# Optimization experiments

Hardware: AMD Instinct MI355X
Metric: run time of the kernel (lower is better)

## Reference

```python
import jax, jax.numpy as jnp
import numpy as np

B, L1, L2, D = 32, 512, 512, 1024


def setup_inputs() -> dict:
    key = jax.random.key(0)
    k1, k2, k3, k4 = jax.random.split(key, 4)
    v1 = jax.random.normal(k1, (B, L1, D), dtype=jnp.float32)
    v2 = jax.random.normal(k2, (B, L2, D), dtype=jnp.float32)
    # row/column is fully masked (which would NaN the softmax).
    v1_mask = jax.random.uniform(k3, (B, L1)) < 0.2
    v2_mask = jax.random.uniform(k4, (B, L2)) < 0.2
    return {"v1": v1, "v2": v2, "v1_mask": v1_mask, "v2_mask": v2_mask}


def reference(v1, v2, v1_mask, v2_mask):
    # similarity: [B, L1, L2]
    sim = jnp.einsum("bid,bjd->bij", v1, v2)
    neg_inf = jnp.float32(-jnp.inf)
    # softmax over v2 positions (dim=2), masking padded v2 columns
    v1_v2_attn = jax.nn.softmax(
        jnp.where(v2_mask[:, None, :], neg_inf, sim), axis=2)
    # softmax over v1 positions (dim=1), masking padded v1 rows
    v2_v1_attn = jax.nn.softmax(
        jnp.where(v1_mask[:, :, None], neg_inf, sim), axis=1)
    attended_v1 = jnp.einsum("bij,bjd->bid", v1_v2_attn, v2)  # [B,L1,D]
    attended_v2 = jnp.einsum("bij,bid->bjd", v2_v1_attn, v1)  # [B,L2,D]
    attended_v1 = jnp.where(v1_mask[:, :, None], 0.0, attended_v1)
    attended_v2 = jnp.where(v2_mask[:, :, None], 0.0, attended_v2)
    return attended_v1, attended_v2
```

## Files before the change

### kernel.cpp

```cpp
#include <hip/hip_runtime.h>
#include <stdint.h>


#define Bn 32
#define Ln 512
#define Dn 1024

typedef __attribute__((ext_vector_type(4))) float f32x4;
typedef __attribute__((ext_vector_type(4))) unsigned short u16x4;
typedef __attribute__((ext_vector_type(8))) unsigned short u16x8;
typedef __attribute__((ext_vector_type(8))) __bf16 bf16x8;

union bfcast { u16x8 u; bf16x8 b; };

__device__ __forceinline__ unsigned short f2bf(float f) {
  unsigned int u = __float_as_uint(f);
  u += 0x7FFFu + ((u >> 16) & 1u);
  return (unsigned short)(u >> 16);
}

__device__ __forceinline__ void async_cp16(const void* g, void* l) {
  __builtin_amdgcn_global_load_lds(
      (__attribute__((address_space(1))) void*)(g),
      (__attribute__((address_space(3))) void*)(l), 16, 0, 0);
}

__device__ __forceinline__ void cvt8(f32x4 x0, f32x4 x1,
                                     bf16x8* hi, bf16x8* lo) {
  float xs[8] = {x0[0], x0[1], x0[2], x0[3], x1[0], x1[1], x1[2], x1[3]};
  u16x8 h, l;
#pragma unroll
  for (int e = 0; e < 8; e++) {
    unsigned int u = __float_as_uint(xs[e]);
    h[e] = (unsigned short)(u >> 16);
    float hf = __uint_as_float(u & 0xFFFF0000u);
    l[e] = (unsigned short)(__float_as_uint(xs[e] - hf) >> 16);
  }
  bfcast ch, cl;
  ch.u = h; cl.u = l;
  *hi = ch.b; *lo = cl.b;
}

__global__ __launch_bounds__(256) void conv_t(
    const float* __restrict__ v1, const float* __restrict__ v2,
    unsigned short* __restrict__ v1t, unsigned short* __restrict__ v2t) {
  __shared__ float tile[64][65];
  const int z = blockIdx.z;
  const float* src = (z < Bn) ? v1 : v2;
  unsigned short* dt = (z < Bn) ? v1t : v2t;
  const int b = z & 31;
  const int d0 = blockIdx.x << 6;
  const int l0 = blockIdx.y << 6;
  const int tid = threadIdx.x;
#pragma unroll
  for (int it = 0; it < 4; it++) {
    int lin = (it << 8) + tid;
    int l = lin >> 4;
    int d4 = (lin & 15) << 2;
    f32x4 x = *(const f32x4*)(src + (size_t)(b * Ln + l0 + l) * Dn + d0 + d4);
    tile[l][d4] = x[0]; tile[l][d4 + 1] = x[1];
    tile[l][d4 + 2] = x[2]; tile[l][d4 + 3] = x[3];
  }
  __syncthreads();
#pragma unroll
  for (int it = 0; it < 4; it++) {
    int lin = (it << 8) + tid;
    int d = lin >> 4;
    int l4 = (lin & 15) << 2;
    u16x4 o;
    o[0] = f2bf(tile[l4][d]);     o[1] = f2bf(tile[l4 + 1][d]);
    o[2] = f2bf(tile[l4 + 2][d]); o[3] = f2bf(tile[l4 + 3][d]);
    *(u16x4*)(dt + (size_t)(b * Dn + d0 + d) * Ln + l0 + l4) = o;
  }
}

__global__ __launch_bounds__(256) void sim_gemm_split(
    const float* __restrict__ V1, const float* __restrict__ V2,
    float* __restrict__ C) {
  __shared__ float As[128 * 32];
  __shared__ float Bs[128 * 32];
  const int b = blockIdx.z;
  const float* Ab = V1 + (size_t)b * Ln * Dn;
  const float* Bb = V2 + (size_t)b * Ln * Dn;
  float* Cb = C + (size_t)b * Ln * Ln;
  const int m0 = blockIdx.y << 7;
  const int n0 = blockIdx.x << 7;
  const int tid = threadIdx.x;
  const int lane = tid & 63;
  const int wave = tid >> 6;
  const int wrow = (wave >> 1) << 6;
  const int wcol = (wave & 1) << 6;

  const int srow = lane >> 3;
  const int scol = ((lane & 7) ^ srow) << 2;
  const float* ga = Ab + (size_t)(m0 + (wave << 5) + srow) * Dn + scol;
  const float* gb = Bb + (size_t)(n0 + (wave << 5) + srow) * Dn + scol;

  const int r = lane & 15;
  const int q = lane >> 4;

  const f32x4 zero4 = {0.f, 0.f, 0.f, 0.f};
  f32x4 acc[4][4];
#pragma unroll
  for (int i = 0; i < 4; i++)
#pragma unroll
    for (int j = 0; j < 4; j++) acc[i][j] = zero4;

  for (int k0 = 0; k0 < Dn; k0 += 32) {
    __syncthreads();
#pragma unroll
    for (int j = 0; j < 4; j++) {
      async_cp16(ga + k0 + j * 8 * Dn, As + ((wave << 5) + j * 8) * 32);
      async_cp16(gb + k0 + j * 8 * Dn, Bs + ((wave << 5) + j * 8) * 32);
    }
    __syncthreads();
    bf16x8 ah[4], al[4], bh[4], bl[4];
#pragma unroll
    for (int t = 0; t < 4; t++) {
      int ra = wrow + (t << 4) + r;
      f32x4 x0 = *(const f32x4*)(As + ra * 32 + ((((q << 1)    ) ^ (ra & 7)) << 2));
      f32x4 x1 = *(const f32x4*)(As + ra * 32 + ((((q << 1) | 1) ^ (ra & 7)) << 2));
      cvt8(x0, x1, &ah[t], &al[t]);
      int rb = wcol + (t << 4) + r;
      f32x4 y0 = *(const f32x4*)(Bs + rb * 32 + ((((q << 1)    ) ^ (rb & 7)) << 2));
      f32x4 y1 = *(const f32x4*)(Bs + rb * 32 + ((((q << 1) | 1) ^ (rb & 7)) << 2));
      cvt8(y0, y1, &bh[t], &bl[t]);
    }
#pragma unroll
    for (int tm = 0; tm < 4; tm++)
#pragma unroll
      for (int tn = 0; tn < 4; tn++) {
        acc[tm][tn] = __builtin_amdgcn_mfma_f32_16x16x32_bf16(
            ah[tm], bh[tn], acc[tm][tn], 0, 0, 0);
        acc[tm][tn] = __builtin_amdgcn_mfma_f32_16x16x32_bf16(
            ah[tm], bl[tn], acc[tm][tn], 0, 0, 0);
        acc[tm][tn] = __builtin_amdgcn_mfma_f32_16x16x32_bf16(
            al[tm], bh[tn], acc[tm][tn], 0, 0, 0);
      }
  }

#pragma unroll
  for (int tm = 0; tm < 4; tm++) {
    int rowb = m0 + wrow + (tm << 4) + (q << 2);
#pragma unroll
    for (int reg = 0; reg < 4; reg++) {
      int row = rowb + reg;
#pragma unroll
      for (int tn = 0; tn < 4; tn++) {
        int col = n0 + wcol + (tn << 4) + r;
        Cb[(size_t)row * Ln + col] = acc[tm][tn][reg];
      }
    }
  }
}

__global__ __launch_bounds__(256) void gemm_nt(
    const unsigned short* __restrict__ A, const unsigned short* __restrict__ Bm,
    float* __restrict__ C, const int* __restrict__ rowmask,
    int M, int N, int K) {
  __shared__ unsigned short As[128 * 32];
  __shared__ unsigned short Bs[128 * 32];
  const int b = blockIdx.z;
  const unsigned short* Ab = A + (size_t)b * M * K;
  const unsigned short* Bb = Bm + (size_t)b * N * K;
  float* Cb = C + (size_t)b * M * N;
  const int m0 = blockIdx.y << 7;
  const int n0 = blockIdx.x << 7;
  const int tid = threadIdx.x;
  const int lane = tid & 63;
  const int wave = tid >> 6;
  const int wrow = (wave >> 1) << 6;
  const int wcol = (wave & 1) << 6;

  const int srow = tid >> 2;
  const int skof = (tid & 3) << 3;
  const unsigned short* ga0 = Ab + (size_t)(m0 + srow) * K + skof;
  const unsigned short* ga1 = Ab + (size_t)(m0 + 64 + srow) * K + skof;
  const unsigned short* gb0 = Bb + (size_t)(n0 + srow) * K + skof;
  const unsigned short* gb1 = Bb + (size_t)(n0 + 64 + srow) * K + skof;

  const int r = lane & 15;
  const int q = lane >> 4;

  const f32x4 zero4 = {0.f, 0.f, 0.f, 0.f};
  f32x4 acc[4][4];
#pragma unroll
  for (int i = 0; i < 4; i++)
#pragma unroll
    for (int j = 0; j < 4; j++) acc[i][j] = zero4;

  for (int k0 = 0; k0 < K; k0 += 32) {
    __syncthreads();
    async_cp16(ga0 + k0, As + (wave << 9));
    async_cp16(ga1 + k0, As + 2048 + (wave << 9));
    async_cp16(gb0 + k0, Bs + (wave << 9));
    async_cp16(gb1 + k0, Bs + 2048 + (wave << 9));
    __syncthreads();
    bf16x8 af[4], bf[4];
#pragma unroll
    for (int t = 0; t < 4; t++) {
      af[t] = *(const bf16x8*)(As + ((wrow + (t << 4) + r) << 5) + (q << 3));
      bf[t] = *(const bf16x8*)(Bs + ((wcol + (t << 4) + r) << 5) + (q << 3));
    }
#pragma unroll
    for (int tm = 0; tm < 4; tm++)
#pragma unroll
      for (int tn = 0; tn < 4; tn++)
        acc[tm][tn] = __builtin_amdgcn_mfma_f32_16x16x32_bf16(
            af[tm], bf[tn], acc[tm][tn], 0, 0, 0);
  }

  const int* mb = rowmask ? rowmask + b * M : (const int*)0;
#pragma unroll
  for (int tm = 0; tm < 4; tm++) {
    int rowb = m0 + wrow + (tm << 4) + (q << 2);
#pragma unroll
    for (int reg = 0; reg < 4; reg++) {
      int row = rowb + reg;
      float mz = (mb && mb[row]) ? 0.f : 1.f;
#pragma unroll
      for (int tn = 0; tn < 4; tn++) {
        int col = n0 + wcol + (tn << 4) + r;
        Cb[(size_t)row * N + col] = acc[tm][tn][reg] * mz;
      }
    }
  }
}

__global__ __launch_bounds__(256) void row_softmax(
    const float* __restrict__ sim, const int* __restrict__ v2m,
    unsigned short* __restrict__ A1) {
  const int row = (blockIdx.x << 2) + (threadIdx.x >> 6);
  const int lane = threadIdx.x & 63;
  const int b = row >> 9;
  const float* s = sim + (size_t)row * Ln;
  const int* mk = v2m + (b << 9);
  const float NEGINF = -__builtin_inff();
  float v[8];
  float mx = NEGINF;
#pragma unroll
  for (int t = 0; t < 8; t++) {
    int j = lane + (t << 6);
    float x = mk[j] ? NEGINF : s[j];
    v[t] = x;
    mx = fmaxf(mx, x);
  }
#pragma unroll
  for (int off = 32; off > 0; off >>= 1) mx = fmaxf(mx, __shfl_xor(mx, off));
  float sum = 0.f;
#pragma unroll
  for (int t = 0; t < 8; t++) {
    float e = (v[t] > NEGINF) ? __expf(v[t] - mx) : 0.f;
    v[t] = e;
    sum += e;
  }
#pragma unroll
  for (int off = 32; off > 0; off >>= 1) sum += __shfl_xor(sum, off);
  float rs = 1.f / sum;
  unsigned short* o = A1 + (size_t)row * Ln;
#pragma unroll
  for (int t = 0; t < 8; t++) o[lane + (t << 6)] = f2bf(v[t] * rs);
}

__global__ __launch_bounds__(256) void csm_part(
    const float* __restrict__ sim, const int* __restrict__ v1m,
    float* __restrict__ pmax, float* __restrict__ psum) {
  __shared__ float sm[4][64], ss[4][64];
  const int b = blockIdx.z;
  const int ic = blockIdx.y;
  const int i0 = ic << 6;
  const int j0 = blockIdx.x << 6;
  const int tx = threadIdx.x & 63;
  const int ty = threadIdx.x >> 6;
  const float* S = sim + (size_t)b * (Ln * Ln) + j0 + tx;
  const int* mk = v1m + (b << 9) + i0;
  const float NEGINF = -__builtin_inff();
  float x[16];
#pragma unroll
  for (int k = 0; k < 16; k++) {
    int il = (k << 2) + ty;
    float v = S[(size_t)(i0 + il) * Ln];
    x[k] = mk[il] ? NEGINF : v;
  }
  float m = NEGINF;
#pragma unroll
  for (int k = 0; k < 16; k++) m = fmaxf(m, x[k]);
  float s = 0.f;
#pragma unroll
  for (int k = 0; k < 16; k++) s += (x[k] > NEGINF) ? __expf(x[k] - m) : 0.f;
  sm[ty][tx] = m;
  ss[ty][tx] = s;
  __syncthreads();
  if (ty == 0) {
    float M = fmaxf(fmaxf(sm[0][tx], sm[1][tx]), fmaxf(sm[2][tx], sm[3][tx]));
    float Sv = 0.f;
#pragma unroll
    for (int p = 0; p < 4; p++)
      Sv += (sm[p][tx] > NEGINF) ? ss[p][tx] * __expf(sm[p][tx] - M) : 0.f;
    int idx = (((b << 3) + ic) << 9) + j0 + tx;
    pmax[idx] = M;
    psum[idx] = Sv;
  }
}

__global__ __launch_bounds__(256) void csm_comb(
    const float* __restrict__ pmax, const float* __restrict__ psum,
    float* __restrict__ cmax, float* __restrict__ crs) {
  const int col = (blockIdx.x << 8) + threadIdx.x;
  const int b = col >> 9;
  const int j = col & 511;
  const float NEGINF = -__builtin_inff();
  float mm[8], sv[8];
#pragma unroll
  for (int p = 0; p < 8; p++) {
    int idx = (((b << 3) + p) << 9) + j;
    mm[p] = pmax[idx];
    sv[p] = psum[idx];
  }
  float M = NEGINF;
#pragma unroll
  for (int p = 0; p < 8; p++) M = fmaxf(M, mm[p]);
  float Sv = 0.f;
#pragma unroll
  for (int p = 0; p < 8; p++)
    Sv += (mm[p] > NEGINF) ? sv[p] * __expf(mm[p] - M) : 0.f;
  cmax[col] = M;
  crs[col] = 1.f / Sv;
}

__global__ __launch_bounds__(256) void csm_write(
    const float* __restrict__ sim, const int* __restrict__ v1m,
    const float* __restrict__ cmax, const float* __restrict__ crs,
    unsigned short* __restrict__ A2t) {
  __shared__ float cm[64], cr[64];
  __shared__ unsigned short Tc[64][66];
  const int b = blockIdx.z;
  const int i0 = blockIdx.y << 6;
  const int j0 = blockIdx.x << 6;
  const int tx = threadIdx.x & 63;
  const int ty = threadIdx.x >> 6;
  if (threadIdx.x < 64) {
    cm[threadIdx.x] = cmax[(b << 9) + j0 + threadIdx.x];
    cr[threadIdx.x] = crs[(b << 9) + j0 + threadIdx.x];
  }
  __syncthreads();
  const float* S = sim + (size_t)b * (Ln * Ln) + j0 + tx;
  const int* mk = v1m + (b << 9) + i0;
  const float cmx = cm[tx];
  const float cs = cr[tx];
#pragma unroll
  for (int k = 0; k < 16; k++) {
    int il = (k << 2) + ty;
    float x = S[(size_t)(i0 + il) * Ln];
    float e = mk[il] ? 0.f : __expf(x - cmx) * cs;
    Tc[tx][il] = f2bf(e);
  }
  __syncthreads();
  unsigned short* o = A2t + ((size_t)(b << 9) + j0) * Ln + i0;
#pragma unroll
  for (int t = 0; t < 4; t++) {
    int c = (t << 8) + (int)threadIdx.x;
    int j = c >> 4;
    int ch = c & 15;
    u16x4 v;
    v[0] = Tc[j][(ch << 2)];     v[1] = Tc[j][(ch << 2) + 1];
    v[2] = Tc[j][(ch << 2) + 2]; v[3] = Tc[j][(ch << 2) + 3];
    *(u16x4*)(o + (size_t)j * Ln + (ch << 2)) = v;
  }
}

extern "C" void kernel_launch(void* const* d_in, const int* in_sizes, int n_in,
                              void* d_out, int out_size, void* d_ws,
                              size_t ws_size, hipStream_t stream) {
  (void)in_sizes; (void)n_in; (void)out_size; (void)ws_size;
  const float* v1 = (const float*)d_in[0];
  const float* v2 = (const float*)d_in[1];
  const int* v1m = (const int*)d_in[2];
  const int* v2m = (const int*)d_in[3];
  float* out1 = (float*)d_out;
  float* out2 = out1 + (size_t)Bn * Ln * Dn;

  char* ws = (char*)d_ws;
  const size_t Mi = 1048576;
  unsigned short* v1t = (unsigned short*)(ws);
  unsigned short* v2t = (unsigned short*)(ws + 32 * Mi);
  float* sim = (float*)(ws + 64 * Mi);
  unsigned short* A1 = (unsigned short*)(ws + 96 * Mi);
  unsigned short* A2t = (unsigned short*)(ws + 112 * Mi);
  float* pmax = (float*)(ws + 128 * Mi);
  float* psum = (float*)(ws + 128 * Mi + 512 * 1024);
  float* cmax = (float*)(ws + 129 * Mi);
  float* crs = (float*)(ws + 129 * Mi + 64 * 1024);

  dim3 blk(256);
  conv_t<<<dim3(16, 8, 64), blk, 0, stream>>>(v1, v2, v1t, v2t);
  sim_gemm_split<<<dim3(4, 4, 32), blk, 0, stream>>>(v1, v2, sim);
  row_softmax<<<dim3(4096), blk, 0, stream>>>(sim, v2m, A1);
  csm_part<<<dim3(8, 8, 32), blk, 0, stream>>>(sim, v1m, pmax, psum);
  csm_comb<<<dim3(64), blk, 0, stream>>>(pmax, psum, cmax, crs);
  csm_write<<<dim3(8, 8, 32), blk, 0, stream>>>(sim, v1m, cmax, crs, A2t);
  gemm_nt<<<dim3(8, 4, 32), blk, 0, stream>>>(A1, v2t, out1, v1m,
                                              512, 1024, 512);
  gemm_nt<<<dim3(8, 4, 32), blk, 0, stream>>>(A2t, v1t, out2, v2m,
                                              512, 1024, 512);
}
```

Measured before the change: 424.8 us.

## Presplit bf16 hi/lo in conversion pass and fuse softmax stats into sim GEMM

The conversion kernel now also writes swizzled bf16 hi/lo splits of v1 and v2. The similarity GEMM therefore loads ready bf16 pairs instead of converting fp32 tiles in its inner loop. The GEMM epilogue computes per-tile row and column max/sum partials, replacing the separate row_softmax and csm_part passes over the sim matrix. A combined stats kernel and a single normalization kernel then write both A1 and A2t in one read of sim, and the two output GEMMs are merged into one launch. This cuts kernel launches and sim re-reads, at the cost of writing and reading extra hi/lo buffers and adding epilogue work.

```diff
diff --git a/kernel.cpp b/kernel.cpp
--- a/kernel.cpp
+++ b/kernel.cpp
@@ -11,8 +11,6 @@
 typedef __attribute__((ext_vector_type(8))) unsigned short u16x8;
 typedef __attribute__((ext_vector_type(8))) __bf16 bf16x8;
 
-union bfcast { u16x8 u; bf16x8 b; };
-
 __device__ __forceinline__ unsigned short f2bf(float f) {
   unsigned int u = __float_as_uint(f);
   u += 0x7FFFu + ((u >> 16) & 1u);
@@ -25,33 +23,22 @@
       (__attribute__((address_space(3))) void*)(l), 16, 0, 0);
 }
 
-__device__ __forceinline__ void cvt8(f32x4 x0, f32x4 x1,
-                                     bf16x8* hi, bf16x8* lo) {
-  float xs[8] = {x0[0], x0[1], x0[2], x0[3], x1[0], x1[1], x1[2], x1[3]};
-  u16x8 h, l;
-#pragma unroll
-  for (int e = 0; e < 8; e++) {
-    unsigned int u = __float_as_uint(xs[e]);
-    h[e] = (unsigned short)(u >> 16);
-    float hf = __uint_as_float(u & 0xFFFF0000u);
-    l[e] = (unsigned short)(__float_as_uint(xs[e] - hf) >> 16);
-  }
-  bfcast ch, cl;
-  ch.u = h; cl.u = l;
-  *hi = ch.b; *lo = cl.b;
-}
-
-__global__ __launch_bounds__(256) void conv_t(
+__global__ __launch_bounds__(256) void conv_split(
     const float* __restrict__ v1, const float* __restrict__ v2,
-    unsigned short* __restrict__ v1t, unsigned short* __restrict__ v2t) {
+    unsigned short* __restrict__ v1t, unsigned short* __restrict__ v2t,
+    unsigned short* __restrict__ v1h, unsigned short* __restrict__ v1l,
+    unsigned short* __restrict__ v2h, unsigned short* __restrict__ v2l) {
   __shared__ float tile[64][65];
   const int z = blockIdx.z;
   const float* src = (z < Bn) ? v1 : v2;
   unsigned short* dt = (z < Bn) ? v1t : v2t;
+  unsigned short* dh = (z < Bn) ? v1h : v2h;
+  unsigned short* dl = (z < Bn) ? v1l : v2l;
   const int b = z & 31;
   const int d0 = blockIdx.x << 6;
   const int l0 = blockIdx.y << 6;
   const int tid = threadIdx.x;
+  const size_t bo = (size_t)b * Ln * Dn;
 #pragma unroll
   for (int it = 0; it < 4; it++) {
     int lin = (it << 8) + tid;
@@ -60,6 +47,19 @@
     f32x4 x = *(const f32x4*)(src + (size_t)(b * Ln + l0 + l) * Dn + d0 + d4);
     tile[l][d4] = x[0]; tile[l][d4 + 1] = x[1];
     tile[l][d4 + 2] = x[2]; tile[l][d4 + 3] = x[3];
+    u16x4 h4, lo4;
+#pragma unroll
+    for (int e = 0; e < 4; e++) {
+      unsigned int u = __float_as_uint(x[e]);
+      h4[e] = (unsigned short)(u >> 16);
+      float hf = __uint_as_float(u & 0xFFFF0000u);
+      lo4[e] = (unsigned short)(__float_as_uint(x[e] - hf) >> 16);
+    }
+    int gl = l0 + l;
+    int sd = (d0 + d4) ^ (((gl >> 1) & 3) << 3);
+    size_t off = bo + (size_t)gl * Dn + sd;
+    *(u16x4*)(dh + off) = h4;
+    *(u16x4*)(dl + off) = lo4;
   }
   __syncthreads();
 #pragma unroll
@@ -74,15 +74,16 @@
   }
 }
 
-__global__ __launch_bounds__(256) void sim_gemm_split(
-    const float* __restrict__ V1, const float* __restrict__ V2,
-    float* __restrict__ C) {
-  __shared__ float As[128 * 32];
-  __shared__ float Bs[128 * 32];
+__global__ __launch_bounds__(256) void sim_gemm(
+    const unsigned short* __restrict__ Ahg, const unsigned short* __restrict__ Alg,
+    const unsigned short* __restrict__ Bhg, const unsigned short* __restrict__ Blg,
+    float* __restrict__ C, const int* __restrict__ v1m,
+    const int* __restrict__ v2m,
+    float* __restrict__ pmaxR, float* __restrict__ psumR,
+    float* __restrict__ pmaxC, float* __restrict__ psumC) {
+  __shared__ unsigned short sAh[128 * 32], sAl[128 * 32];
+  __shared__ unsigned short sBh[128 * 32], sBl[128 * 32];
   const int b = blockIdx.z;
-  const float* Ab = V1 + (size_t)b * Ln * Dn;
-  const float* Bb = V2 + (size_t)b * Ln * Dn;
-  float* Cb = C + (size_t)b * Ln * Ln;
   const int m0 = blockIdx.y << 7;
   const int n0 = blockIdx.x << 7;
   const int tid = threadIdx.x;
@@ -90,14 +91,16 @@
   const int wave = tid >> 6;
   const int wrow = (wave >> 1) << 6;
   const int wcol = (wave & 1) << 6;
-
-  const int srow = lane >> 3;
-  const int scol = ((lane & 7) ^ srow) << 2;
-  const float* ga = Ab + (size_t)(m0 + (wave << 5) + srow) * Dn + scol;
-  const float* gb = Bb + (size_t)(n0 + (wave << 5) + srow) * Dn + scol;
-
   const int r = lane & 15;
   const int q = lane >> 4;
+  const int srow = tid >> 2;
+  const int skof = (tid & 3) << 3;
+  const size_t bo = (size_t)b * Ln * Dn;
+  const unsigned short* gah = Ahg + bo + (size_t)(m0 + srow) * Dn + skof;
+  const unsigned short* gal = Alg + bo + (size_t)(m0 + srow) * Dn + skof;
+  const unsigned short* gbh = Bhg + bo + (size_t)(n0 + srow) * Dn + skof;
+  const unsigned short* gbl = Blg + bo + (size_t)(n0 + srow) * Dn + skof;
+  const int ldsw = wave << 9;
 
   const f32x4 zero4 = {0.f, 0.f, 0.f, 0.f};
   f32x4 acc[4][4];
@@ -108,23 +111,26 @@
 
   for (int k0 = 0; k0 < Dn; k0 += 32) {
     __syncthreads();
-#pragma unroll
-    for (int j = 0; j < 4; j++) {
-      async_cp16(ga + k0 + j * 8 * Dn, As + ((wave << 5) + j * 8) * 32);
-      async_cp16(gb + k0 + j * 8 * Dn, Bs + ((wave << 5) + j * 8) * 32);
-    }
+    async_cp16(gah + k0, sAh + ldsw);
+    async_cp16(gah + (size_t)64 * Dn + k0, sAh + 2048 + ldsw);
+    async_cp16(gal + k0, sAl + ldsw);
+    async_cp16(gal + (size_t)64 * Dn + k0, sAl + 2048 + ldsw);
+    async_cp16(gbh + k0, sBh + ldsw);
+    async_cp16(gbh + (size_t)64 * Dn + k0, sBh + 2048 + ldsw);
+    async_cp16(gbl + k0, sBl + ldsw);
+    async_cp16(gbl + (size_t)64 * Dn + k0, sBl + 2048 + ldsw);
     __syncthreads();
     bf16x8 ah[4], al[4], bh[4], bl[4];
 #pragma unroll
     for (int t = 0; t < 4; t++) {
       int ra = wrow + (t << 4) + r;
-      f32x4 x0 = *(const f32x4*)(As + ra * 32 + ((((q << 1)    ) ^ (ra & 7)) << 2));
-      f32x4 x1 = *(const f32x4*)(As + ra * 32 + ((((q << 1) | 1) ^ (ra & 7)) << 2));
-      cvt8(x0, x1, &ah[t], &al[t]);
+      int sa = (ra << 5) + ((q ^ ((ra >> 1) & 3)) << 3);
+      ah[t] = *(const bf16x8*)(sAh + sa);
+      al[t] = *(const bf16x8*)(sAl + sa);
       int rb = wcol + (t << 4) + r;
-      f32x4 y0 = *(const f32x4*)(Bs + rb * 32 + ((((q << 1)    ) ^ (rb & 7)) << 2));
-      f32x4 y1 = *(const f32x4*)(Bs + rb * 32 + ((((q << 1) | 1) ^ (rb & 7)) << 2));
-      cvt8(y0, y1, &bh[t], &bl[t]);
+      int sb = (rb << 5) + ((q ^ ((rb >> 1) & 3)) << 3);
+      bh[t] = *(const bf16x8*)(sBh + sb);
+      bl[t] = *(const bf16x8*)(sBl + sb);
     }
 #pragma unroll
     for (int tm = 0; tm < 4; tm++)
@@ -139,6 +145,7 @@
       }
   }
 
+  float* Cb = C + (size_t)b * Ln * Ln;
 #pragma unroll
   for (int tm = 0; tm < 4; tm++) {
     int rowb = m0 + wrow + (tm << 4) + (q << 2);
@@ -152,18 +159,179 @@
       }
     }
   }
-}
-
-__global__ __launch_bounds__(256) void gemm_nt(
-    const unsigned short* __restrict__ A, const unsigned short* __restrict__ Bm,
-    float* __restrict__ C, const int* __restrict__ rowmask,
-    int M, int N, int K) {
+
+  const int* mkr = v1m + (b << 9);
+  const int* mkc = v2m + (b << 9);
+  const float NEGINF = -__builtin_inff();
+  unsigned cmb = 0;
+#pragma unroll
+  for (int tn = 0; tn < 4; tn++)
+    cmb |= (mkc[n0 + wcol + (tn << 4) + r] ? 1u : 0u) << tn;
+  unsigned rmb = 0;
+#pragma unroll
+  for (int t2 = 0; t2 < 16; t2++)
+    rmb |= (mkr[m0 + wrow + ((t2 >> 2) << 4) + (q << 2) + (t2 & 3)] ? 1u : 0u)
+           << t2;
+
+  const int nsub = (n0 + wcol) >> 6;
+#pragma unroll
+  for (int tm = 0; tm < 4; tm++) {
+#pragma unroll
+    for (int reg = 0; reg < 4; reg++) {
+      float m = NEGINF;
+#pragma unroll
+      for (int tn = 0; tn < 4; tn++)
+        if (!((cmb >> tn) & 1)) m = fmaxf(m, acc[tm][tn][reg]);
+#pragma unroll
+      for (int off = 1; off < 16; off <<= 1)
+        m = fmaxf(m, __shfl_xor(m, off));
+      float s = 0.f;
+#pragma unroll
+      for (int tn = 0; tn < 4; tn++)
+        if (!((cmb >> tn) & 1)) s += __expf(acc[tm][tn][reg] - m);
+#pragma unroll
+      for (int off = 1; off < 16; off <<= 1) s += __shfl_xor(s, off);
+      if (r == 0) {
+        int row = m0 + wrow + (tm << 4) + (q << 2) + reg;
+        int idx = (((b << 3) + nsub) << 9) + row;
+        pmaxR[idx] = m;
+        psumR[idx] = s;
+      }
+    }
+  }
+
+  const int msub = (m0 + wrow) >> 6;
+#pragma unroll
+  for (int tn = 0; tn < 4; tn++) {
+    float m = NEGINF;
+#pragma unroll
+    for (int tm = 0; tm < 4; tm++)
+#pragma unroll
+      for (int reg = 0; reg < 4; reg++)
+        if (!((rmb >> ((tm << 2) + reg)) & 1))
+          m = fmaxf(m, acc[tm][tn][reg]);
+    m = fmaxf(m, __shfl_xor(m, 16));
+    m = fmaxf(m, __shfl_xor(m, 32));
+    float s = 0.f;
+#pragma unroll
+    for (int tm = 0; tm < 4; tm++)
+#pragma unroll
+      for (int reg = 0; reg < 4; reg++)
+        if (!((rmb >> ((tm << 2) + reg)) & 1))
+          s += __expf(acc[tm][tn][reg] - m);
+    s += __shfl_xor(s, 16);
+    s += __shfl_xor(s, 32);
+    if (q == 0) {
+      int col = n0 + wcol + (tn << 4) + r;
+      int idx = (((b << 3) + msub) << 9) + col;
+      pmaxC[idx] = m;
+      psumC[idx] = s;
+    }
+  }
+}
+
+__global__ __launch_bounds__(256) void comb(
+    const float* __restrict__ pmaxR, const float* __restrict__ psumR,
+    const float* __restrict__ pmaxC, const float* __restrict__ psumC,
+    float* __restrict__ rowmax, float* __restrict__ rowrs,
+    float* __restrict__ colmax, float* __restrict__ colrs) {
+  const int id = (blockIdx.x << 8) + threadIdx.x;
+  const int side = id >> 14;
+  const int x = id & 16383;
+  const float* pm = side ? pmaxC : pmaxR;
+  const float* ps = side ? psumC : psumR;
+  const int bq = x >> 9;
+  const int j = x & 511;
+  const float NEGINF = -__builtin_inff();
+  float mm[8], sv[8];
+#pragma unroll
+  for (int p = 0; p < 8; p++) {
+    int idx = (((bq << 3) + p) << 9) + j;
+    mm[p] = pm[idx];
+    sv[p] = ps[idx];
+  }
+  float M = NEGINF;
+#pragma unroll
+  for (int p = 0; p < 8; p++) M = fmaxf(M, mm[p]);
+  float S = 0.f;
+#pragma unroll
+  for (int p = 0; p < 8; p++)
+    S += (mm[p] > NEGINF) ? sv[p] * __expf(mm[p] - M) : 0.f;
+  float rs = 1.f / S;
+  if (side) { colmax[x] = M; colrs[x] = rs; }
+  else      { rowmax[x] = M; rowrs[x] = rs; }
+}
+
+__global__ __launch_bounds__(256) void norm_write(
+    const float* __restrict__ sim, const int* __restrict__ v1m,
+    const int* __restrict__ v2m,
+    const float* __restrict__ rowmax, const float* __restrict__ rowrs,
+    const float* __restrict__ colmax, const float* __restrict__ colrs,
+    unsigned short* __restrict__ A1, unsigned short* __restrict__ A2t) {
+  __shared__ unsigned short Tc[64][66];
+  __shared__ float rm[64], rr[64], cmx[64], crx[64];
+  const int b = blockIdx.z;
+  const int i0 = blockIdx.y << 6;
+  const int j0 = blockIdx.x << 6;
+  const int tid = threadIdx.x;
+  if (tid < 64) {
+    cmx[tid] = colmax[(b << 9) + j0 + tid];
+    crx[tid] = colrs[(b << 9) + j0 + tid];
+  } else if (tid < 128) {
+    int t = tid - 64;
+    rm[t] = rowmax[(b << 9) + i0 + t];
+    rr[t] = rowrs[(b << 9) + i0 + t];
+  }
+  __syncthreads();
+  const int tx = tid & 63;
+  const int ty = tid >> 6;
+  const float* S = sim + (size_t)b * (Ln * Ln) + j0 + tx;
+  const int* mr = v1m + (b << 9) + i0;
+  const int jm = v2m[(b << 9) + j0 + tx];
+  const float cm0 = cmx[tx];
+  const float cs0 = crx[tx];
+  unsigned short* A1b = A1 + ((size_t)((b << 9) + i0)) * Ln + j0;
+#pragma unroll
+  for (int k = 0; k < 16; k++) {
+    int il = (k << 2) + ty;
+    float x = S[(size_t)(i0 + il) * Ln];
+    float e1 = jm ? 0.f : __expf(x - rm[il]) * rr[il];
+    A1b[(size_t)il * Ln + tx] = f2bf(e1);
+    float e2 = mr[il] ? 0.f : __expf(x - cm0) * cs0;
+    Tc[tx][il] = f2bf(e2);
+  }
+  __syncthreads();
+  unsigned short* o = A2t + ((size_t)((b << 9) + j0)) * Ln + i0;
+#pragma unroll
+  for (int t = 0; t < 4; t++) {
+    int c = (t << 8) + tid;
+    int j = c >> 4;
+    int ch = c & 15;
+    u16x4 v;
+    v[0] = Tc[j][(ch << 2)];     v[1] = Tc[j][(ch << 2) + 1];
+    v[2] = Tc[j][(ch << 2) + 2]; v[3] = Tc[j][(ch << 2) + 3];
+    *(u16x4*)(o + (size_t)j * Ln + (ch << 2)) = v;
+  }
+}
+
+__global__ __launch_bounds__(256) void gemm_nt2(
+    const unsigned short* __restrict__ A1g, const unsigned short* __restrict__ A2tg,
+    const unsigned short* __restrict__ v2t, const unsigned short* __restrict__ v1t,
+    float* __restrict__ out1, float* __restrict__ out2,
+    const int* __restrict__ v1m, const int* __restrict__ v2m) {
+  const int Mv = 512, Nv = 1024, Kv = 512;
   __shared__ unsigned short As[128 * 32];
   __shared__ unsigned short Bs[128 * 32];
-  const int b = blockIdx.z;
-  const unsigned short* Ab = A + (size_t)b * M * K;
-  const unsigned short* Bb = Bm + (size_t)b * N * K;
-  float* Cb = C + (size_t)b * M * N;
+  const int z = blockIdx.z;
+  const int b = z & 31;
+  const int w2 = z >> 5;
+  const unsigned short* A = w2 ? A2tg : A1g;
+  const unsigned short* Bm = w2 ? v1t : v2t;
+  float* C = w2 ? out2 : out1;
+  const int* rowmask = w2 ? v2m : v1m;
+  const unsigned short* Ab = A + (size_t)b * Mv * Kv;
+  const unsigned short* Bb = Bm + (size_t)b * Nv * Kv;
+  float* Cb = C + (size_t)b * Mv * Nv;
   const int m0 = blockIdx.y << 7;
   const int n0 = blockIdx.x << 7;
   const int tid = threadIdx.x;
@@ -174,10 +342,10 @@
 
   const int srow = tid >> 2;
   const int skof = (tid & 3) << 3;
-  const unsigned short* ga0 = Ab + (size_t)(m0 + srow) * K + skof;
-  const unsigned short* ga1 = Ab + (size_t)(m0 + 64 + srow) * K + skof;
-  const unsigned short* gb0 = Bb + (size_t)(n0 + srow) * K + skof;
-  const unsigned short* gb1 = Bb + (size_t)(n0 + 64 + srow) * K + skof;
+  const unsigned short* ga0 = Ab + (size_t)(m0 + srow) * Kv + skof;
+  const unsigned short* ga1 = Ab + (size_t)(m0 + 64 + srow) * Kv + skof;
+  const unsigned short* gb0 = Bb + (size_t)(n0 + srow) * Kv + skof;
+  const unsigned short* gb1 = Bb + (size_t)(n0 + 64 + srow) * Kv + skof;
 
   const int r = lane & 15;
   const int q = lane >> 4;
@@ -189,183 +357,41 @@
 #pragma unroll
     for (int j = 0; j < 4; j++) acc[i][j] = zero4;
 
-  for (int k0 = 0; k0 < K; k0 += 32) {
+  for (int k0 = 0; k0 < Kv; k0 += 32) {
     __syncthreads();
     async_cp16(ga0 + k0, As + (wave << 9));
     async_cp16(ga1 + k0, As + 2048 + (wave << 9));
     async_cp16(gb0 + k0, Bs + (wave << 9));
     async_cp16(gb1 + k0, Bs + 2048 + (wave << 9));
     __syncthreads();
-    bf16x8 af[4], bf[4];
+    bf16x8 af[4], bfr[4];
 #pragma unroll
     for (int t = 0; t < 4; t++) {
       af[t] = *(const bf16x8*)(As + ((wrow + (t << 4) + r) << 5) + (q << 3));
-      bf[t] = *(const bf16x8*)(Bs + ((wcol + (t << 4) + r) << 5) + (q << 3));
+      bfr[t] = *(const bf16x8*)(Bs + ((wcol + (t << 4) + r) << 5) + (q << 3));
     }
 #pragma unroll
     for (int tm = 0; tm < 4; tm++)
 #pragma unroll
       for (int tn = 0; tn < 4; tn++)
         acc[tm][tn] = __builtin_amdgcn_mfma_f32_16x16x32_bf16(
-            af[tm], bf[tn], acc[tm][tn], 0, 0, 0);
-  }
-
-  const int* mb = rowmask ? rowmask + b * M : (const int*)0;
+            af[tm], bfr[tn], acc[tm][tn], 0, 0, 0);
+  }
+
+  const int* mb = rowmask + b * Mv;
 #pragma unroll
   for (int tm = 0; tm < 4; tm++) {
     int rowb = m0 + wrow + (tm << 4) + (q << 2);
 #pragma unroll
     for (int reg = 0; reg < 4; reg++) {
       int row = rowb + reg;
-      float mz = (mb && mb[row]) ? 0.f : 1.f;
+      float mz = mb[row] ? 0.f : 1.f;
 #pragma unroll
       for (int tn = 0; tn < 4; tn++) {
         int col = n0 + wcol + (tn << 4) + r;
-        Cb[(size_t)row * N + col] = acc[tm][tn][reg] * mz;
+        Cb[(size_t)row * Nv + col] = acc[tm][tn][reg] * mz;
       }
     }
-  }
-}
-
-__global__ __launch_bounds__(256) void row_softmax(
-    const float* __restrict__ sim, const int* __restrict__ v2m,
-    unsigned short* __restrict__ A1) {
-  const int row = (blockIdx.x << 2) + (threadIdx.x >> 6);
-  const int lane = threadIdx.x & 63;
-  const int b = row >> 9;
-  const float* s = sim + (size_t)row * Ln;
-  const int* mk = v2m + (b << 9);
-  const float NEGINF = -__builtin_inff();
-  float v[8];
-  float mx = NEGINF;
-#pragma unroll
-  for (int t = 0; t < 8; t++) {
-    int j = lane + (t << 6);
-    float x = mk[j] ? NEGINF : s[j];
-    v[t] = x;
-    mx = fmaxf(mx, x);
-  }
-#pragma unroll
-  for (int off = 32; off > 0; off >>= 1) mx = fmaxf(mx, __shfl_xor(mx, off));
-  float sum = 0.f;
-#pragma unroll
-  for (int t = 0; t < 8; t++) {
-    float e = (v[t] > NEGINF) ? __expf(v[t] - mx) : 0.f;
-    v[t] = e;
-    sum += e;
-  }
-#pragma unroll
-  for (int off = 32; off > 0; off >>= 1) sum += __shfl_xor(sum, off);
-  float rs = 1.f / sum;
-  unsigned short* o = A1 + (size_t)row * Ln;
-#pragma unroll
-  for (int t = 0; t < 8; t++) o[lane + (t << 6)] = f2bf(v[t] * rs);
-}
-
-__global__ __launch_bounds__(256) void csm_part(
-    const float* __restrict__ sim, const int* __restrict__ v1m,
-    float* __restrict__ pmax, float* __restrict__ psum) {
-  __shared__ float sm[4][64], ss[4][64];
-  const int b = blockIdx.z;
-  const int ic = blockIdx.y;
-  const int i0 = ic << 6;
-  const int j0 = blockIdx.x << 6;
-  const int tx = threadIdx.x & 63;
-  const int ty = threadIdx.x >> 6;
-  const float* S = sim + (size_t)b * (Ln * Ln) + j0 + tx;
-  const int* mk = v1m + (b << 9) + i0;
-  const float NEGINF = -__builtin_inff();
-  float x[16];
-#pragma unroll
-  for (int k = 0; k < 16; k++) {
-    int il = (k << 2) + ty;
-    float v = S[(size_t)(i0 + il) * Ln];
-    x[k] = mk[il] ? NEGINF : v;
-  }
-  float m = NEGINF;
-#pragma unroll
-  for (int k = 0; k < 16; k++) m = fmaxf(m, x[k]);
-  float s = 0.f;
-#pragma unroll
-  for (int k = 0; k < 16; k++) s += (x[k] > NEGINF) ? __expf(x[k] - m) : 0.f;
-  sm[ty][tx] = m;
-  ss[ty][tx] = s;
-  __syncthreads();
-  if (ty == 0) {
-    float M = fmaxf(fmaxf(sm[0][tx], sm[1][tx]), fmaxf(sm[2][tx], sm[3][tx]));
-    float Sv = 0.f;
-#pragma unroll
-    for (int p = 0; p < 4; p++)
-      Sv += (sm[p][tx] > NEGINF) ? ss[p][tx] * __expf(sm[p][tx] - M) : 0.f;
-    int idx = (((b << 3) + ic) << 9) + j0 + tx;
-    pmax[idx] = M;
-    psum[idx] = Sv;
-  }
-}
-
-__global__ __launch_bounds__(256) void csm_comb(
-    const float* __restrict__ pmax, const float* __restrict__ psum,
-    float* __restrict__ cmax, float* __restrict__ crs) {
-  const int col = (blockIdx.x << 8) + threadIdx.x;
-  const int b = col >> 9;
-  const int j = col & 511;
-  const float NEGINF = -__builtin_inff();
-  float mm[8], sv[8];
-#pragma unroll
-  for (int p = 0; p < 8; p++) {
-    int idx = (((b << 3) + p) << 9) + j;
-    mm[p] = pmax[idx];
-    sv[p] = psum[idx];
-  }
-  float M = NEGINF;
-#pragma unroll
-  for (int p = 0; p < 8; p++) M = fmaxf(M, mm[p]);
-  float Sv = 0.f;
-#pragma unroll
-  for (int p = 0; p < 8; p++)
-    Sv += (mm[p] > NEGINF) ? sv[p] * __expf(mm[p] - M) : 0.f;
-  cmax[col] = M;
-  crs[col] = 1.f / Sv;
-}
-
-__global__ __launch_bounds__(256) void csm_write(
-    const float* __restrict__ sim, const int* __restrict__ v1m,
-    const float* __restrict__ cmax, const float* __restrict__ crs,
-    unsigned short* __restrict__ A2t) {
-  __shared__ float cm[64], cr[64];
-  __shared__ unsigned short Tc[64][66];
-  const int b = blockIdx.z;
-  const int i0 = blockIdx.y << 6;
-  const int j0 = blockIdx.x << 6;
-  const int tx = threadIdx.x & 63;
-  const int ty = threadIdx.x >> 6;
-  if (threadIdx.x < 64) {
-    cm[threadIdx.x] = cmax[(b << 9) + j0 + threadIdx.x];
-    cr[threadIdx.x] = crs[(b << 9) + j0 + threadIdx.x];
-  }
-  __syncthreads();
-  const float* S = sim + (size_t)b * (Ln * Ln) + j0 + tx;
-  const int* mk = v1m + (b << 9) + i0;
-  const float cmx = cm[tx];
-  const float cs = cr[tx];
-#pragma unroll
-  for (int k = 0; k < 16; k++) {
-    int il = (k << 2) + ty;
-    float x = S[(size_t)(i0 + il) * Ln];
-    float e = mk[il] ? 0.f : __expf(x - cmx) * cs;
-    Tc[tx][il] = f2bf(e);
-  }
-  __syncthreads();
-  unsigned short* o = A2t + ((size_t)(b << 9) + j0) * Ln + i0;
-#pragma unroll
-  for (int t = 0; t < 4; t++) {
-    int c = (t << 8) + (int)threadIdx.x;
-    int j = c >> 4;
-    int ch = c & 15;
-    u16x4 v;
-    v[0] = Tc[j][(ch << 2)];     v[1] = Tc[j][(ch << 2) + 1];
-    v[2] = Tc[j][(ch << 2) + 2]; v[3] = Tc[j][(ch << 2) + 3];
-    *(u16x4*)(o + (size_t)j * Ln + (ch << 2)) = v;
   }
 }
 
@@ -384,23 +410,32 @@
   const size_t Mi = 1048576;
   unsigned short* v1t = (unsigned short*)(ws);
   unsigned short* v2t = (unsigned short*)(ws + 32 * Mi);
-  float* sim = (float*)(ws + 64 * Mi);
-  unsigned short* A1 = (unsigned short*)(ws + 96 * Mi);
-  unsigned short* A2t = (unsigned short*)(ws + 112 * Mi);
-  float* pmax = (float*)(ws + 128 * Mi);
-  float* psum = (float*)(ws + 128 * Mi + 512 * 1024);
-  float* cmax = (float*)(ws + 129 * Mi);
-  float* crs = (float*)(ws + 129 * Mi + 64 * 1024);
+  unsigned short* v1h = (unsigned short*)(ws + 64 * Mi);
+  unsigned short* v2h = (unsigned short*)(ws + 96 * Mi);
+  unsigned short* v1l = (unsigned short*)(ws + 128 * Mi);
+  unsigned short* v2l = (unsigned short*)(ws + 160 * Mi);
+  float* sim = (float*)(ws + 192 * Mi);
+  unsigned short* A1 = (unsigned short*)(ws + 64 * Mi);
+  unsigned short* A2t = (unsigned short*)(ws + 80 * Mi);
+  float* pmaxR = (float*)(ws + 224 * Mi);
+  float* psumR = (float*)(ws + 224 * Mi + 512 * 1024);
+  float* pmaxC = (float*)(ws + 225 * Mi);
+  float* psumC = (float*)(ws + 225 * Mi + 512 * 1024);
+  float* rowmax = (float*)(ws + 226 * Mi);
+  float* rowrs = (float*)(ws + 226 * Mi + 64 * 1024);
+  float* colmax = (float*)(ws + 226 * Mi + 128 * 1024);
+  float* colrs = (float*)(ws + 226 * Mi + 192 * 1024);
 
   dim3 blk(256);
-  conv_t<<<dim3(16, 8, 64), blk, 0, stream>>>(v1, v2, v1t, v2t);
-  sim_gemm_split<<<dim3(4, 4, 32), blk, 0, stream>>>(v1, v2, sim);
-  row_softmax<<<dim3(4096), blk, 0, stream>>>(sim, v2m, A1);
-  csm_part<<<dim3(8, 8, 32), blk, 0, stream>>>(sim, v1m, pmax, psum);
-  csm_comb<<<dim3(64), blk, 0, stream>>>(pmax, psum, cmax, crs);
-  csm_write<<<dim3(8, 8, 32), blk, 0, stream>>>(sim, v1m, cmax, crs, A2t);
-  gemm_nt<<<dim3(8, 4, 32), blk, 0, stream>>>(A1, v2t, out1, v1m,
-                                              512, 1024, 512);
-  gemm_nt<<<dim3(8, 4, 32), blk, 0, stream>>>(A2t, v1t, out2, v2m,
-                                              512, 1024, 512);
-}
+  conv_split<<<dim3(16, 8, 64), blk, 0, stream>>>(v1, v2, v1t, v2t,
+                                                  v1h, v1l, v2h, v2l);
+  sim_gemm<<<dim3(4, 4, 32), blk, 0, stream>>>(v1h, v1l, v2h, v2l, sim,
+                                               v1m, v2m, pmaxR, psumR,
+                                               pmaxC, psumC);
+  comb<<<dim3(128), blk, 0, stream>>>(pmaxR, psumR, pmaxC, psumC,
+                                      rowmax, rowrs, colmax, colrs);
+  norm_write<<<dim3(8, 8, 32), blk, 0, stream>>>(sim, v1m, v2m, rowmax, rowrs,
+                                                 colmax, colrs, A1, A2t);
+  gemm_nt2<<<dim3(8, 4, 64), blk, 0, stream>>>(A1, A2t, v2t, v1t,
+                                               out1, out2, v1m, v2m);
+}
```

After: 434.0 us. 2.2% more time.
